# Kernel optimization log

Measured on AMD Instinct MI355X. Metric: run time of the kernel, lower is better.

Reference implementation:

```python
import jax, jax.numpy as jnp
import numpy as np
import math

B, S, D, H = 64, 512, 768, 12
HS = D // H  # head size = 64


def setup_inputs() -> dict:
    key = jax.random.key(0)
    ks = jax.random.split(key, 8)
    scale = 1.0 / math.sqrt(D)
    return {
        "from_tensor": jax.random.normal(ks[0], (B, S, D), jnp.float32),
        "to_tensor": jax.random.normal(ks[1], (B, S, D), jnp.float32),
        "Wq": jax.random.normal(ks[2], (D, D), jnp.float32) * scale,
        "bq": jax.random.normal(ks[3], (D,), jnp.float32) * 0.02,
        "Wk": jax.random.normal(ks[4], (D, D), jnp.float32) * scale,
        "bk": jax.random.normal(ks[5], (D,), jnp.float32) * 0.02,
        "Wv": jax.random.normal(ks[6], (D, D), jnp.float32) * scale,
        "bv": jax.random.normal(ks[7], (D,), jnp.float32) * 0.02,
    }


def _split_heads(x):
    # [B, S, D] -> [B, H, S, HS]
    return x.reshape(B, S, H, HS).transpose(0, 2, 1, 3)


def reference(from_tensor, to_tensor, Wq, bq, Wk, bk, Wv, bv):
    q = _split_heads(from_tensor @ Wq + bq)
    k = _split_heads(to_tensor @ Wk + bk)
    v = _split_heads(to_tensor @ Wv + bv)
    scores = jnp.einsum("bhqd,bhkd->bhqk", q, k) / math.sqrt(HS)
    probs = jax.nn.softmax(scores, axis=-1)
    out = jnp.einsum("bhqk,bhkd->bhqd", probs, v)
    return out.transpose(0, 2, 1, 3).reshape(B, S, D)
```

## Files before the change

### kernel.cpp

```cpp
#include <hip/hip_runtime.h>
#include <hip/hip_bf16.h>

#define GAS __attribute__((address_space(1)))
#define LAS __attribute__((address_space(3)))

typedef __attribute__((ext_vector_type(8))) short   bf16x8;
typedef __attribute__((ext_vector_type(4))) float   f32x4;
typedef __attribute__((ext_vector_type(16))) float  f32x16;
typedef __attribute__((ext_vector_type(4))) float   f4;
typedef __attribute__((ext_vector_type(8))) short   s8v;
typedef __attribute__((ext_vector_type(2))) unsigned int u32x2;
typedef __attribute__((ext_vector_type(4))) unsigned int u32x4;

#define NB  64
#define NS  512
#define ND  768
#define NH  12
#define NHS 64
#define NM  (NB*NS)
#define NBH (NB*NH)

#define QSCALE 0.18033688011112042f

__device__ __forceinline__ unsigned short f2bf(float x){
  unsigned int u = __float_as_uint(x);
  u += 0x7fffu + ((u >> 16) & 1u);
  return (unsigned short)(u >> 16);
}

__device__ __forceinline__ f32x4 mfma16(bf16x8 a, bf16x8 b, f32x4 c){
  return __builtin_amdgcn_mfma_f32_16x16x32_bf16(a, b, c, 0, 0, 0);
}

__device__ __forceinline__ f32x16 mfma32(bf16x8 a, bf16x8 b, f32x16 c){
  return __builtin_amdgcn_mfma_f32_32x32x16_bf16(a, b, c, 0, 0, 0);
}

__device__ __forceinline__ unsigned int cvtpk(float lo, float hi){
  unsigned int r;
  asm("v_cvt_pk_bf16_f32 %0, %1, %2" : "=v"(r) : "v"(lo), "v"(hi));
  return r;
}

__device__ __forceinline__ bf16x8 u2b(u32x4 u){
  union { u32x4 a; bf16x8 b; } c; c.a = u; return c.b;
}

__global__ void cvt_x(const float* __restrict__ from_t, const float* __restrict__ to_t,
                      short* __restrict__ fb, short* __restrict__ tb){
  int v = blockIdx.x * 256 + threadIdx.x;
  const int NG = NM * ND / 8;
  const float* s; short* d;
  if (v < NG){ s = from_t; d = fb; } else { s = to_t; d = tb; v -= NG; }
  f4 a = ((const f4*)s)[(long)v * 2];
  f4 b = ((const f4*)s)[(long)v * 2 + 1];
  s8v o;
  o[0]=(short)f2bf(a[0]); o[1]=(short)f2bf(a[1]); o[2]=(short)f2bf(a[2]); o[3]=(short)f2bf(a[3]);
  o[4]=(short)f2bf(b[0]); o[5]=(short)f2bf(b[1]); o[6]=(short)f2bf(b[2]); o[7]=(short)f2bf(b[3]);
  ((s8v*)d)[v] = o;
}

__global__ void cvt_w(const float* __restrict__ Wq, const float* __restrict__ Wk,
                      const float* __restrict__ Wv, short* __restrict__ Wt){
  int i = blockIdx.x * 256 + threadIdx.x;
  int mat = i / (ND*ND);
  int rem = i - mat * (ND*ND);
  int k = rem / ND;
  int n = rem - k * ND;
  const float* W = (mat == 0) ? Wq : (mat == 1 ? Wk : Wv);
  Wt[(long)mat*ND*ND + (long)n*ND + k] = (short)f2bf(W[rem]);
}

__global__ __launch_bounds__(512, 2)
void qkv_gemm(const short* __restrict__ Xf, const short* __restrict__ Xt,
              const short* __restrict__ Wt,
              const float* __restrict__ bq, const float* __restrict__ bk,
              const float* __restrict__ bv,
              short* __restrict__ Qw, short* __restrict__ Kw, short* __restrict__ Vtw){
  __shared__ short smem[49152];

  int bid = blockIdx.x;
  int wg  = (bid & 7) * 144 + (bid >> 3);
  int mat = wg / 384;
  int r   = wg - mat * 384;
  int mt  = r / 3;
  int nt  = r - mt * 3;

  const short* A  = (mat == 0) ? Xf : Xt;
  const short* Wp = Wt + (long)mat * ND * ND;

  int t_ = threadIdx.x, wv = t_ >> 6, l = t_ & 63, g = l >> 4, c = l & 15;
  int wm = wv >> 2, wn = wv & 3;
  int m0 = mt * 256, n0 = nt * 256;

  short* As[3] = { smem, smem + 8192, smem + 16384 };
  short* Bs[3] = { smem + 24576, smem + 32768, smem + 40960 };

  auto stage = [&](int kt, short* Ab, short* Bb, int ci){
    int chunk = ci * 8 + wv;
    int ch = chunk & 15;
    int idx = ch * 64 + l;
    int row = idx >> 2, slot = idx & 3;
    int kcol = kt * 32 + ((slot ^ ((row >> 1) & 3)) << 3);
    if (chunk < 16){
      const short* gp = A + (long)(m0 + row) * ND + kcol;
      __builtin_amdgcn_global_load_lds((const GAS unsigned int*)gp,
                                       (LAS unsigned int*)(Ab + ch * 512), 16, 0, 0);
    } else {
      const short* gp = Wp + (long)(n0 + row) * ND + kcol;
      __builtin_amdgcn_global_load_lds((const GAS unsigned int*)gp,
                                       (LAS unsigned int*)(Bb + ch * 512), 16, 0, 0);
    }
  };

  f32x4 zero = {0.f, 0.f, 0.f, 0.f};
  f32x4 acc[8][4];
  #pragma unroll
  for (int i = 0; i < 8; ++i)
    #pragma unroll
    for (int j = 0; j < 4; ++j) acc[i][j] = zero;

  #pragma unroll
  for (int ci = 0; ci < 4; ++ci) stage(0, As[0], Bs[0], ci);
  #pragma unroll
  for (int ci = 0; ci < 4; ++ci) stage(1, As[1], Bs[1], ci);

  auto step = [&](const short* Asl, const short* Bsl, short* An, short* Bn, int t){
    if (t == 23) asm volatile("s_waitcnt vmcnt(0)" ::: "memory");
    else         asm volatile("s_waitcnt vmcnt(4)" ::: "memory");
    __builtin_amdgcn_s_barrier();
    bf16x8 af[8], bfr[4];
    #pragma unroll
    for (int ms = 0; ms < 4; ++ms){
      int row = wm * 128 + ms * 16 + c;
      af[ms] = *(const bf16x8*)(Asl + row * 32 + ((g ^ ((row >> 1) & 3)) << 3));
    }
    if (t < 22) stage(t + 2, An, Bn, 0);
    #pragma unroll
    for (int ns = 0; ns < 4; ++ns){
      int row = wn * 64 + ns * 16 + c;
      bfr[ns] = *(const bf16x8*)(Bsl + row * 32 + ((g ^ ((row >> 1) & 3)) << 3));
    }
    if (t < 22) stage(t + 2, An, Bn, 1);
    #pragma unroll
    for (int ms = 4; ms < 8; ++ms){
      int row = wm * 128 + ms * 16 + c;
      af[ms] = *(const bf16x8*)(Asl + row * 32 + ((g ^ ((row >> 1) & 3)) << 3));
    }
    if (t < 22){ stage(t + 2, An, Bn, 2); stage(t + 2, An, Bn, 3); }
    __builtin_amdgcn_s_setprio(1);
    #pragma unroll
    for (int ms = 0; ms < 8; ++ms)
      #pragma unroll
      for (int ns = 0; ns < 4; ++ns)
        acc[ms][ns] = mfma16(af[ms], bfr[ns], acc[ms][ns]);
    __builtin_amdgcn_s_setprio(0);
  };

  for (int it = 0; it < 8; ++it){
    int t = it * 3;
    step(As[0], Bs[0], As[2], Bs[2], t);
    step(As[1], Bs[1], As[0], Bs[0], t + 1);
    step(As[2], Bs[2], As[1], Bs[1], t + 2);
  }

  __builtin_amdgcn_s_barrier();

  int n0g = n0 + wn * 64;
  const float* bias = (mat == 0) ? bq : (mat == 1 ? bk : bv);
  float bb[4];
  #pragma unroll
  for (int ns = 0; ns < 4; ++ns) bb[ns] = bias[n0g + ns * 16 + c];
  short* chunk = smem + wv * 4096;
  int hq = n0g >> 6;

  if (mat < 2){
    short* O = (mat == 0) ? Qw : Kw;
    float scl = (mat == 0) ? QSCALE : 1.0f;
    #pragma unroll
    for (int sp = 0; sp < 2; ++sp){
      #pragma unroll
      for (int msl = 0; msl < 4; ++msl){
        #pragma unroll
        for (int ns = 0; ns < 4; ++ns){
          int col = ns * 16 + c;
          #pragma unroll
          for (int i = 0; i < 4; ++i){
            int row = msl * 16 + g * 4 + i;
            chunk[row * 64 + (((col >> 3) ^ (row & 7)) << 3) + (col & 7)] =
                (short)f2bf((acc[sp * 4 + msl][ns][i] + bb[ns]) * scl);
          }
        }
      }
      asm volatile("s_waitcnt lgkmcnt(0)" ::: "memory");
      __builtin_amdgcn_sched_barrier(0);
      #pragma unroll
      for (int rr = 0; rr < 8; ++rr){
        int row = rr * 8 + (l >> 3);
        int slot = l & 7;
        bf16x8 v = *(const bf16x8*)(chunk + row * 64 + ((slot ^ (row & 7)) << 3));
        int m = m0 + wm * 128 + sp * 64 + row;
        int b = m >> 9, s2 = m & 511;
        *(bf16x8*)(O + (((long)(b * NH + hq) * NS + s2) << 6) + slot * 8) = v;
      }
      if (sp == 0){ asm volatile("s_waitcnt lgkmcnt(0)" ::: "memory"); }
    }
  } else {
    #pragma unroll
    for (int sp = 0; sp < 2; ++sp){
      #pragma unroll
      for (int msl = 0; msl < 4; ++msl){
        #pragma unroll
        for (int ns = 0; ns < 4; ++ns){
          int hs = ns * 16 + c;
          #pragma unroll
          for (int i = 0; i < 4; ++i){
            int col = msl * 16 + g * 4 + i;
            chunk[hs * 64 + (((col >> 3) ^ (hs & 7)) << 3) + (col & 7)] =
                (short)f2bf(acc[sp * 4 + msl][ns][i] + bb[ns]);
          }
        }
      }
      asm volatile("s_waitcnt lgkmcnt(0)" ::: "memory");
      __builtin_amdgcn_sched_barrier(0);
      int mbase = m0 + wm * 128 + sp * 64;
      int b = mbase >> 9, s0 = mbase & 511;
      #pragma unroll
      for (int rr = 0; rr < 8; ++rr){
        int hs = rr * 8 + (l >> 3);
        int slot = l & 7;
        bf16x8 v = *(const bf16x8*)(chunk + hs * 64 + ((slot ^ (hs & 7)) << 3));
        *(bf16x8*)(Vtw + (long)((b * NH + hq) * 64 + hs) * NS + s0 + slot * 8) = v;
      }
      if (sp == 0){ asm volatile("s_waitcnt lgkmcnt(0)" ::: "memory"); }
    }
  }
}

__global__ __launch_bounds__(512, 1)
void attn_kernel(const short* __restrict__ Qw, const short* __restrict__ Kw,
                 const short* __restrict__ Vtw, float* __restrict__ out){
  extern __shared__ char smem[];
  short* Ks = (short*)smem;
  short* Vs = (short*)(smem + 65536);

  int bh = blockIdx.x;
  int t = threadIdx.x, wv = t >> 6, l = t & 63;
  int lam = l & 31, hi = l >> 5;
  int r7 = lam & 7;

  const short* Kb = Kw  + (long)bh * NS * NHS;
  const short* Vb = Vtw + (long)bh * NS * NHS;

  #pragma unroll
  for (int it = 0; it < 8; ++it){
    int chunk = it * 8 + wv;
    {
      int idx = chunk * 64 + l;
      int row = idx >> 3, slot = idx & 7;
      const short* gk = Kb + row * 64 + ((slot ^ (row & 7)) * 8);
      __builtin_amdgcn_global_load_lds((const GAS unsigned int*)gk,
                                       (LAS unsigned int*)(Ks + chunk * 512), 16, 0, 0);
    }
    {
      int row = chunk, slot = l;
      const short* gv = Vb + (long)row * NS + (((slot & 56) | ((slot & 7) ^ (row & 7))) * 8);
      __builtin_amdgcn_global_load_lds((const GAS unsigned int*)gv,
                                       (LAS unsigned int*)(Vs + chunk * 512), 16, 0, 0);
    }
  }
  __syncthreads();

  int b = bh / NH, h = bh - b * NH;
  float* outb = out + (long)b * NS * ND + (long)h * 64;

  for (int qt = 0; qt < 2; ++qt){
    int q0 = wv * 64 + qt * 32;
    const short* Qb = Qw + (((long)bh * NS + q0 + lam) << 6) + hi * 8;
    bf16x8 qf[4];
    #pragma unroll
    for (int dk = 0; dk < 4; ++dk) qf[dk] = *(const bf16x8*)(Qb + dk * 16);

    f32x16 o0, o1;
    #pragma unroll
    for (int j = 0; j < 16; ++j){ o0[j] = 0.f; o1[j] = 0.f; }
    float m_run = -1e30f, lsum = 0.f;

    #pragma unroll
    for (int ch = 0; ch < 16; ++ch){
      f32x16 s;
      #pragma unroll
      for (int j = 0; j < 16; ++j) s[j] = 0.f;
      const char* kbase = (const char*)Ks + (ch * 32 + lam) * 128;
      #pragma unroll
      for (int dk = 0; dk < 4; ++dk){
        bf16x8 kf = *(const bf16x8*)(kbase + (((hi + 2 * dk) ^ r7) << 4));
        s = mfma32(kf, qf[dk], s);
      }

      float t8[8], t4[4];
      #pragma unroll
      for (int j = 0; j < 8; ++j) t8[j] = fmaxf(s[j], s[j + 8]);
      #pragma unroll
      for (int j = 0; j < 4; ++j) t4[j] = fmaxf(t8[j], t8[j + 4]);
      float m1 = fmaxf(fmaxf(t4[0], t4[1]), fmaxf(t4[2], t4[3]));
      float pmax = fmaxf(m1, __shfl_xor(m1, 32));
      if (__any(pmax > m_run + 8.0f)){
        float mnew = fmaxf(m_run, pmax);
        float cf = exp2f(m_run - mnew);
        lsum *= cf;
        #pragma unroll
        for (int j = 0; j < 16; ++j){ o0[j] *= cf; o1[j] *= cf; }
        m_run = mnew;
      }
      float p[16];
      #pragma unroll
      for (int j = 0; j < 16; ++j) p[j] = exp2f(s[j] - m_run);
      float a8[8], a4[4];
      #pragma unroll
      for (int j = 0; j < 8; ++j) a8[j] = p[j] + p[j + 8];
      #pragma unroll
      for (int j = 0; j < 4; ++j) a4[j] = a8[j] + a8[j + 4];
      lsum += (a4[0] + a4[1]) + (a4[2] + a4[3]);

      unsigned int w[8];
      #pragma unroll
      for (int rr = 0; rr < 8; ++rr) w[rr] = cvtpk(p[2 * rr], p[2 * rr + 1]);
      unsigned int y0 = (unsigned int)__shfl_xor((int)(hi ? w[0] : w[2]), 32);
      unsigned int y1 = (unsigned int)__shfl_xor((int)(hi ? w[1] : w[3]), 32);
      unsigned int y2 = (unsigned int)__shfl_xor((int)(hi ? w[4] : w[6]), 32);
      unsigned int y3 = (unsigned int)__shfl_xor((int)(hi ? w[5] : w[7]), 32);
      u32x4 fa, fb;
      if (hi){
        fa[0] = y0;   fa[1] = y1;   fa[2] = w[2]; fa[3] = w[3];
        fb[0] = y2;   fb[1] = y3;   fb[2] = w[6]; fb[3] = w[7];
      } else {
        fa[0] = w[0]; fa[1] = w[1]; fa[2] = y0;   fa[3] = y1;
        fb[0] = w[4]; fb[1] = w[5]; fb[2] = y2;   fb[3] = y3;
      }
      bf16x8 pa = u2b(fa), pb = u2b(fb);

      const char* vb0 = (const char*)Vs + lam * 1024;
      const char* vb1 = (const char*)Vs + (32 + lam) * 1024;
      int sl0 = ch * 4 + hi, sl1 = ch * 4 + 2 + hi;
      int sw0 = ((sl0 & 56) | ((sl0 & 7) ^ r7)) << 4;
      int sw1 = ((sl1 & 56) | ((sl1 & 7) ^ r7)) << 4;
      bf16x8 v00 = *(const bf16x8*)(vb0 + sw0);
      bf16x8 v01 = *(const bf16x8*)(vb0 + sw1);
      bf16x8 v10 = *(const bf16x8*)(vb1 + sw0);
      bf16x8 v11 = *(const bf16x8*)(vb1 + sw1);
      o0 = mfma32(v00, pa, o0);
      o0 = mfma32(v01, pb, o0);
      o1 = mfma32(v10, pa, o1);
      o1 = mfma32(v11, pb, o1);
    }

    float lt = lsum + __shfl_xor(lsum, 32);
    float invl = 1.0f / lt;
    float* orow = outb + (long)(q0 + lam) * ND;
    #pragma unroll
    for (int r = 0; r < 4; ++r){
      f4 u0, u1;
      #pragma unroll
      for (int jj = 0; jj < 4; ++jj){
        u0[jj] = o0[4 * r + jj] * invl;
        u1[jj] = o1[4 * r + jj] * invl;
      }
      *(f4*)(orow + 4 * hi + 8 * r)      = u0;
      *(f4*)(orow + 32 + 4 * hi + 8 * r) = u1;
    }
  }
}

extern "C" void kernel_launch(void* const* d_in, const int* in_sizes, int n_in,
                              void* d_out, int out_size, void* d_ws, size_t ws_size,
                              hipStream_t stream){
  const float* from_t = (const float*)d_in[0];
  const float* to_t   = (const float*)d_in[1];
  const float* Wq = (const float*)d_in[2];
  const float* bq = (const float*)d_in[3];
  const float* Wk = (const float*)d_in[4];
  const float* bk = (const float*)d_in[5];
  const float* Wv = (const float*)d_in[6];
  const float* bv = (const float*)d_in[7];

  short* fb  = (short*)d_ws;
  short* tb  = fb  + 25165824;
  short* Wt  = tb  + 25165824;
  short* Qw  = Wt  + 1769472;
  short* Kw  = Qw  + 25165824;
  short* Vtw = Kw  + 25165824;

  cvt_x<<<24576, 256, 0, stream>>>(from_t, to_t, fb, tb);
  cvt_w<<<6912, 256, 0, stream>>>(Wq, Wk, Wv, Wt);
  qkv_gemm<<<1152, 512, 0, stream>>>(fb, tb, Wt, bq, bk, bv, Qw, Kw, Vtw);
  attn_kernel<<<768, 512, 131072, stream>>>(Qw, Kw, Vtw, (float*)d_out);
}
```

Before: 330.9 us.

## Restructure QKV GEMM mainloop into 4-stage ping-pong pipeline with split MFMA phases

Replaces the 3-buffer LDS pipeline with a 4-slot ring (LDS grows to 128KB), prefetching three k-tiles ahead. Each k-step is split into two halves: loads of half the A fragments, issue of the A or B tile prefetch, then 16 MFMAs, with barriers between phases in a ping-pong style. The aim is to hide global-load latency and overlap LDS reads with MFMA, at the cost of more barriers per step and a larger LDS footprint that may limit blocks per CU.

Result: no change. 330.2 us (-0.2%).

```diff
diff --git a/kernel.cpp b/kernel.cpp
--- a/kernel.cpp
+++ b/kernel.cpp
@@ -77,7 +77,7 @@
               const float* __restrict__ bq, const float* __restrict__ bk,
               const float* __restrict__ bv,
               short* __restrict__ Qw, short* __restrict__ Kw, short* __restrict__ Vtw){
-  __shared__ short smem[49152];
+  __shared__ short smem[65536];
 
   int bid = blockIdx.x;
   int wg  = (bid & 7) * 144 + (bid >> 3);
@@ -93,23 +93,18 @@
   int wm = wv >> 2, wn = wv & 3;
   int m0 = mt * 256, n0 = nt * 256;
 
-  short* As[3] = { smem, smem + 8192, smem + 16384 };
-  short* Bs[3] = { smem + 24576, smem + 32768, smem + 40960 };
-
-  auto stage = [&](int kt, short* Ab, short* Bb, int ci){
-    int chunk = ci * 8 + wv;
-    int ch = chunk & 15;
-    int idx = ch * 64 + l;
-    int row = idx >> 2, slot = idx & 3;
-    int kcol = kt * 32 + ((slot ^ ((row >> 1) & 3)) << 3);
-    if (chunk < 16){
-      const short* gp = A + (long)(m0 + row) * ND + kcol;
+  auto stageH = [&](int kt2, int hf){
+    int sl = kt2 & 3;
+    short* base = smem + (hf ? 32768 : 0) + sl * 8192;
+    const short* src = hf ? Wp : A;
+    int r0 = hf ? n0 : m0;
+    #pragma unroll
+    for (int j = 0; j < 2; ++j){
+      int idx = j * 512 + t_;
+      int row = idx >> 2, slot = idx & 3;
+      const short* gp = src + (long)(r0 + row) * ND + kt2 * 32 + ((slot ^ ((row >> 1) & 3)) << 3);
       __builtin_amdgcn_global_load_lds((const GAS unsigned int*)gp,
-                                       (LAS unsigned int*)(Ab + ch * 512), 16, 0, 0);
-    } else {
-      const short* gp = Wp + (long)(n0 + row) * ND + kcol;
-      __builtin_amdgcn_global_load_lds((const GAS unsigned int*)gp,
-                                       (LAS unsigned int*)(Bb + ch * 512), 16, 0, 0);
+                                       (LAS unsigned int*)(base + idx * 8), 16, 0, 0);
     }
   };
 
@@ -120,51 +115,63 @@
     #pragma unroll
     for (int j = 0; j < 4; ++j) acc[i][j] = zero;
 
-  #pragma unroll
-  for (int ci = 0; ci < 4; ++ci) stage(0, As[0], Bs[0], ci);
-  #pragma unroll
-  for (int ci = 0; ci < 4; ++ci) stage(1, As[1], Bs[1], ci);
-
-  auto step = [&](const short* Asl, const short* Bsl, short* An, short* Bn, int t){
-    if (t == 23) asm volatile("s_waitcnt vmcnt(0)" ::: "memory");
-    else         asm volatile("s_waitcnt vmcnt(4)" ::: "memory");
-    __builtin_amdgcn_s_barrier();
-    bf16x8 af[8], bfr[4];
-    #pragma unroll
-    for (int ms = 0; ms < 4; ++ms){
-      int row = wm * 128 + ms * 16 + c;
-      af[ms] = *(const bf16x8*)(Asl + row * 32 + ((g ^ ((row >> 1) & 3)) << 3));
-    }
-    if (t < 22) stage(t + 2, An, Bn, 0);
+  stageH(0, 0); stageH(0, 1);
+  stageH(1, 0); stageH(1, 1);
+  stageH(2, 0); stageH(2, 1);
+  asm volatile("s_waitcnt vmcnt(8)" ::: "memory");
+  __builtin_amdgcn_s_barrier();
+
+  bf16x8 bfr[4];
+  for (int kt = 0; kt < 24; ++kt){
+    int sl = kt & 3;
+    const short* Asl = smem + sl * 8192;
+    const short* Bsl = smem + 32768 + sl * 8192;
+
+    bf16x8 af[4];
+    #pragma unroll
+    for (int i = 0; i < 4; ++i){
+      int row = wm * 128 + i * 16 + c;
+      af[i] = *(const bf16x8*)(Asl + row * 32 + ((g ^ ((row >> 1) & 3)) << 3));
+    }
     #pragma unroll
     for (int ns = 0; ns < 4; ++ns){
       int row = wn * 64 + ns * 16 + c;
       bfr[ns] = *(const bf16x8*)(Bsl + row * 32 + ((g ^ ((row >> 1) & 3)) << 3));
     }
-    if (t < 22) stage(t + 2, An, Bn, 1);
-    #pragma unroll
-    for (int ms = 4; ms < 8; ++ms){
-      int row = wm * 128 + ms * 16 + c;
-      af[ms] = *(const bf16x8*)(Asl + row * 32 + ((g ^ ((row >> 1) & 3)) << 3));
-    }
-    if (t < 22){ stage(t + 2, An, Bn, 2); stage(t + 2, An, Bn, 3); }
+    if (kt < 21) stageH(kt + 3, 0);
+    __builtin_amdgcn_s_barrier();
+    asm volatile("s_waitcnt lgkmcnt(0)" ::: "memory");
+    __builtin_amdgcn_sched_barrier(0);
     __builtin_amdgcn_s_setprio(1);
     #pragma unroll
-    for (int ms = 0; ms < 8; ++ms)
+    for (int i = 0; i < 4; ++i)
       #pragma unroll
       for (int ns = 0; ns < 4; ++ns)
-        acc[ms][ns] = mfma16(af[ms], bfr[ns], acc[ms][ns]);
+        acc[i][ns] = mfma16(af[i], bfr[ns], acc[i][ns]);
     __builtin_amdgcn_s_setprio(0);
-  };
-
-  for (int it = 0; it < 8; ++it){
-    int t = it * 3;
-    step(As[0], Bs[0], As[2], Bs[2], t);
-    step(As[1], Bs[1], As[0], Bs[0], t + 1);
-    step(As[2], Bs[2], As[1], Bs[1], t + 2);
+    __builtin_amdgcn_s_barrier();
+
+    #pragma unroll
+    for (int i = 0; i < 4; ++i){
+      int row = wm * 128 + (4 + i) * 16 + c;
+      af[i] = *(const bf16x8*)(Asl + row * 32 + ((g ^ ((row >> 1) & 3)) << 3));
+    }
+    if (kt < 21) stageH(kt + 3, 1);
+    __builtin_amdgcn_s_barrier();
+    asm volatile("s_waitcnt lgkmcnt(0)" ::: "memory");
+    __builtin_amdgcn_sched_barrier(0);
+    __builtin_amdgcn_s_setprio(1);
+    #pragma unroll
+    for (int i = 0; i < 4; ++i)
+      #pragma unroll
+      for (int ns = 0; ns < 4; ++ns)
+        acc[4 + i][ns] = mfma16(af[i], bfr[ns], acc[4 + i][ns]);
+    __builtin_amdgcn_s_setprio(0);
+    if (kt <= 20)      asm volatile("s_waitcnt vmcnt(8)" ::: "memory");
+    else if (kt == 21) asm volatile("s_waitcnt vmcnt(4)" ::: "memory");
+    else if (kt == 22) asm volatile("s_waitcnt vmcnt(0)" ::: "memory");
+    __builtin_amdgcn_s_barrier();
   }
-
-  __builtin_amdgcn_s_barrier();
 
   int n0g = n0 + wn * 64;
   const float* bias = (mat == 0) ? bq : (mat == 1 ? bk : bv);
```

## Shrink QKV GEMM tiles to 128x128, single-buffer K=64 steps, merge conversion kernels

Applied to the files above, without the earlier changes.

Merges the activation and weight bf16 conversion kernels into one launch. Rewrites the QKV projection GEMM from 256x256 tiles with 512 threads and a triple-buffered K=32 pipeline into 128x128 tiles with 256 threads. The new GEMM uses a single 32KB LDS buffer with K=64 steps and two syncthreads per step, launching four times as many blocks. This trades data reuse and load/compute overlap for higher occupancy and a simpler schedule, and risks exposing global-load latency because loads are no longer prefetched ahead of compute.

Result: slower. 375.2 us (+13.4%).

```diff
diff --git a/kernel.cpp b/kernel.cpp
--- a/kernel.cpp
+++ b/kernel.cpp
@@ -9,7 +9,6 @@
 typedef __attribute__((ext_vector_type(16))) float  f32x16;
 typedef __attribute__((ext_vector_type(4))) float   f4;
 typedef __attribute__((ext_vector_type(8))) short   s8v;
-typedef __attribute__((ext_vector_type(2))) unsigned int u32x2;
 typedef __attribute__((ext_vector_type(4))) unsigned int u32x4;
 
 #define NB  64
@@ -18,7 +17,6 @@
 #define NH  12
 #define NHS 64
 #define NM  (NB*NS)
-#define NBH (NB*NH)
 
 #define QSCALE 0.18033688011112042f
 
@@ -46,125 +44,106 @@
   union { u32x4 a; bf16x8 b; } c; c.a = u; return c.b;
 }
 
-__global__ void cvt_x(const float* __restrict__ from_t, const float* __restrict__ to_t,
-                      short* __restrict__ fb, short* __restrict__ tb){
-  int v = blockIdx.x * 256 + threadIdx.x;
-  const int NG = NM * ND / 8;
-  const float* s; short* d;
-  if (v < NG){ s = from_t; d = fb; } else { s = to_t; d = tb; v -= NG; }
-  f4 a = ((const f4*)s)[(long)v * 2];
-  f4 b = ((const f4*)s)[(long)v * 2 + 1];
-  s8v o;
-  o[0]=(short)f2bf(a[0]); o[1]=(short)f2bf(a[1]); o[2]=(short)f2bf(a[2]); o[3]=(short)f2bf(a[3]);
-  o[4]=(short)f2bf(b[0]); o[5]=(short)f2bf(b[1]); o[6]=(short)f2bf(b[2]); o[7]=(short)f2bf(b[3]);
-  ((s8v*)d)[v] = o;
-}
-
-__global__ void cvt_w(const float* __restrict__ Wq, const float* __restrict__ Wk,
-                      const float* __restrict__ Wv, short* __restrict__ Wt){
-  int i = blockIdx.x * 256 + threadIdx.x;
-  int mat = i / (ND*ND);
-  int rem = i - mat * (ND*ND);
-  int k = rem / ND;
-  int n = rem - k * ND;
-  const float* W = (mat == 0) ? Wq : (mat == 1 ? Wk : Wv);
-  Wt[(long)mat*ND*ND + (long)n*ND + k] = (short)f2bf(W[rem]);
-}
-
-__global__ __launch_bounds__(512, 2)
+__global__ void cvt_all(const float* __restrict__ from_t, const float* __restrict__ to_t,
+                        const float* __restrict__ Wq, const float* __restrict__ Wk,
+                        const float* __restrict__ Wv,
+                        short* __restrict__ fb, short* __restrict__ tb,
+                        short* __restrict__ Wt){
+  int bid = blockIdx.x;
+  if (bid < 24576){
+    int v = bid * 256 + threadIdx.x;
+    const int NG = NM * ND / 8;
+    const float* s; short* d;
+    if (v < NG){ s = from_t; d = fb; } else { s = to_t; d = tb; v -= NG; }
+    f4 a = ((const f4*)s)[(long)v * 2];
+    f4 b = ((const f4*)s)[(long)v * 2 + 1];
+    s8v o;
+    o[0]=(short)f2bf(a[0]); o[1]=(short)f2bf(a[1]); o[2]=(short)f2bf(a[2]); o[3]=(short)f2bf(a[3]);
+    o[4]=(short)f2bf(b[0]); o[5]=(short)f2bf(b[1]); o[6]=(short)f2bf(b[2]); o[7]=(short)f2bf(b[3]);
+    ((s8v*)d)[v] = o;
+  } else {
+    int i = (bid - 24576) * 256 + threadIdx.x;
+    int mat = i / (ND*ND);
+    int rem = i - mat * (ND*ND);
+    int k = rem / ND;
+    int n = rem - k * ND;
+    const float* W = (mat == 0) ? Wq : (mat == 1 ? Wk : Wv);
+    Wt[(long)mat*ND*ND + (long)n*ND + k] = (short)f2bf(W[rem]);
+  }
+}
+
+__global__ __launch_bounds__(256)
 void qkv_gemm(const short* __restrict__ Xf, const short* __restrict__ Xt,
               const short* __restrict__ Wt,
               const float* __restrict__ bq, const float* __restrict__ bk,
               const float* __restrict__ bv,
               short* __restrict__ Qw, short* __restrict__ Kw, short* __restrict__ Vtw){
-  __shared__ short smem[49152];
+  __shared__ short smem[16384];
 
   int bid = blockIdx.x;
-  int wg  = (bid & 7) * 144 + (bid >> 3);
-  int mat = wg / 384;
-  int r   = wg - mat * 384;
-  int mt  = r / 3;
-  int nt  = r - mt * 3;
+  int wg  = (bid & 7) * 576 + (bid >> 3);
+  int mat = wg / 1536;
+  int r   = wg - mat * 1536;
+  int mt  = r / 6;
+  int nt  = r - mt * 6;
 
   const short* A  = (mat == 0) ? Xf : Xt;
   const short* Wp = Wt + (long)mat * ND * ND;
 
   int t_ = threadIdx.x, wv = t_ >> 6, l = t_ & 63, g = l >> 4, c = l & 15;
-  int wm = wv >> 2, wn = wv & 3;
-  int m0 = mt * 256, n0 = nt * 256;
-
-  short* As[3] = { smem, smem + 8192, smem + 16384 };
-  short* Bs[3] = { smem + 24576, smem + 32768, smem + 40960 };
-
-  auto stage = [&](int kt, short* Ab, short* Bb, int ci){
-    int chunk = ci * 8 + wv;
-    int ch = chunk & 15;
-    int idx = ch * 64 + l;
-    int row = idx >> 2, slot = idx & 3;
-    int kcol = kt * 32 + ((slot ^ ((row >> 1) & 3)) << 3);
-    if (chunk < 16){
-      const short* gp = A + (long)(m0 + row) * ND + kcol;
-      __builtin_amdgcn_global_load_lds((const GAS unsigned int*)gp,
-                                       (LAS unsigned int*)(Ab + ch * 512), 16, 0, 0);
-    } else {
-      const short* gp = Wp + (long)(n0 + row) * ND + kcol;
-      __builtin_amdgcn_global_load_lds((const GAS unsigned int*)gp,
-                                       (LAS unsigned int*)(Bb + ch * 512), 16, 0, 0);
+  int wm = wv >> 1, wn = wv & 1;
+  int m0 = mt * 128, n0 = nt * 128;
+
+  auto stage = [&](int kt){
+    #pragma unroll
+    for (int it = 0; it < 4; ++it){
+      int idx = it * 256 + t_;
+      int row = idx >> 3, slot = idx & 7;
+      int kc = kt * 64 + ((slot ^ (row & 7)) << 3);
+      const short* ga = A + (long)(m0 + row) * ND + kc;
+      __builtin_amdgcn_global_load_lds((const GAS unsigned int*)ga,
+                                       (LAS unsigned int*)(smem + idx * 8), 16, 0, 0);
+      const short* gb = Wp + (long)(n0 + row) * ND + kc;
+      __builtin_amdgcn_global_load_lds((const GAS unsigned int*)gb,
+                                       (LAS unsigned int*)(smem + 8192 + idx * 8), 16, 0, 0);
     }
   };
 
   f32x4 zero = {0.f, 0.f, 0.f, 0.f};
-  f32x4 acc[8][4];
+  f32x4 acc[4][4];
   #pragma unroll
-  for (int i = 0; i < 8; ++i)
+  for (int i = 0; i < 4; ++i)
     #pragma unroll
     for (int j = 0; j < 4; ++j) acc[i][j] = zero;
 
-  #pragma unroll
-  for (int ci = 0; ci < 4; ++ci) stage(0, As[0], Bs[0], ci);
-  #pragma unroll
-  for (int ci = 0; ci < 4; ++ci) stage(1, As[1], Bs[1], ci);
-
-  auto step = [&](const short* Asl, const short* Bsl, short* An, short* Bn, int t){
-    if (t == 23) asm volatile("s_waitcnt vmcnt(0)" ::: "memory");
-    else         asm volatile("s_waitcnt vmcnt(4)" ::: "memory");
-    __builtin_amdgcn_s_barrier();
-    bf16x8 af[8], bfr[4];
+  stage(0);
+  for (int kt = 0; kt < 12; ++kt){
+    __syncthreads();
+    bf16x8 af[4][2], bfr[4][2];
     #pragma unroll
     for (int ms = 0; ms < 4; ++ms){
-      int row = wm * 128 + ms * 16 + c;
-      af[ms] = *(const bf16x8*)(Asl + row * 32 + ((g ^ ((row >> 1) & 3)) << 3));
-    }
-    if (t < 22) stage(t + 2, An, Bn, 0);
+      int row = wm * 64 + ms * 16 + c;
+      #pragma unroll
+      for (int kk = 0; kk < 2; ++kk)
+        af[ms][kk] = *(const bf16x8*)(smem + row * 64 + (((kk * 4 + g) ^ (row & 7)) << 3));
+    }
     #pragma unroll
     for (int ns = 0; ns < 4; ++ns){
       int row = wn * 64 + ns * 16 + c;
-      bfr[ns] = *(const bf16x8*)(Bsl + row * 32 + ((g ^ ((row >> 1) & 3)) << 3));
-    }
-    if (t < 22) stage(t + 2, An, Bn, 1);
-    #pragma unroll
-    for (int ms = 4; ms < 8; ++ms){
-      int row = wm * 128 + ms * 16 + c;
-      af[ms] = *(const bf16x8*)(Asl + row * 32 + ((g ^ ((row >> 1) & 3)) << 3));
-    }
-    if (t < 22){ stage(t + 2, An, Bn, 2); stage(t + 2, An, Bn, 3); }
-    __builtin_amdgcn_s_setprio(1);
-    #pragma unroll
-    for (int ms = 0; ms < 8; ++ms)
-      #pragma unroll
-      for (int ns = 0; ns < 4; ++ns)
-        acc[ms][ns] = mfma16(af[ms], bfr[ns], acc[ms][ns]);
-    __builtin_amdgcn_s_setprio(0);
-  };
-
-  for (int it = 0; it < 8; ++it){
-    int t = it * 3;
-    step(As[0], Bs[0], As[2], Bs[2], t);
-    step(As[1], Bs[1], As[0], Bs[0], t + 1);
-    step(As[2], Bs[2], As[1], Bs[1], t + 2);
-  }
-
-  __builtin_amdgcn_s_barrier();
+      #pragma unroll
+      for (int kk = 0; kk < 2; ++kk)
+        bfr[ns][kk] = *(const bf16x8*)(smem + 8192 + row * 64 + (((kk * 4 + g) ^ (row & 7)) << 3));
+    }
+    #pragma unroll
+    for (int kk = 0; kk < 2; ++kk)
+      #pragma unroll
+      for (int ms = 0; ms < 4; ++ms)
+        #pragma unroll
+        for (int ns = 0; ns < 4; ++ns)
+          acc[ms][ns] = mfma16(af[ms][kk], bfr[ns][kk], acc[ms][ns]);
+    __syncthreads();
+    if (kt < 11) stage(kt + 1);
+  }
 
   int n0g = n0 + wn * 64;
   const float* bias = (mat == 0) ? bq : (mat == 1 ? bk : bv);
@@ -173,66 +152,56 @@
   for (int ns = 0; ns < 4; ++ns) bb[ns] = bias[n0g + ns * 16 + c];
   short* chunk = smem + wv * 4096;
   int hq = n0g >> 6;
+  int mbase = m0 + wm * 64;
+  int b = mbase >> 9, s0 = mbase & 511;
 
   if (mat < 2){
     short* O = (mat == 0) ? Qw : Kw;
     float scl = (mat == 0) ? QSCALE : 1.0f;
     #pragma unroll
-    for (int sp = 0; sp < 2; ++sp){
-      #pragma unroll
-      for (int msl = 0; msl < 4; ++msl){
+    for (int msl = 0; msl < 4; ++msl){
+      #pragma unroll
+      for (int ns = 0; ns < 4; ++ns){
+        int col = ns * 16 + c;
         #pragma unroll
-        for (int ns = 0; ns < 4; ++ns){
-          int col = ns * 16 + c;
-          #pragma unroll
-          for (int i = 0; i < 4; ++i){
-            int row = msl * 16 + g * 4 + i;
-            chunk[row * 64 + (((col >> 3) ^ (row & 7)) << 3) + (col & 7)] =
-                (short)f2bf((acc[sp * 4 + msl][ns][i] + bb[ns]) * scl);
-          }
+        for (int i = 0; i < 4; ++i){
+          int row = msl * 16 + g * 4 + i;
+          chunk[row * 64 + (((col >> 3) ^ (row & 7)) << 3) + (col & 7)] =
+              (short)f2bf((acc[msl][ns][i] + bb[ns]) * scl);
         }
       }
-      asm volatile("s_waitcnt lgkmcnt(0)" ::: "memory");
-      __builtin_amdgcn_sched_barrier(0);
-      #pragma unroll
-      for (int rr = 0; rr < 8; ++rr){
-        int row = rr * 8 + (l >> 3);
-        int slot = l & 7;
-        bf16x8 v = *(const bf16x8*)(chunk + row * 64 + ((slot ^ (row & 7)) << 3));
-        int m = m0 + wm * 128 + sp * 64 + row;
-        int b = m >> 9, s2 = m & 511;
-        *(bf16x8*)(O + (((long)(b * NH + hq) * NS + s2) << 6) + slot * 8) = v;
-      }
-      if (sp == 0){ asm volatile("s_waitcnt lgkmcnt(0)" ::: "memory"); }
+    }
+    asm volatile("s_waitcnt lgkmcnt(0)" ::: "memory");
+    __builtin_amdgcn_sched_barrier(0);
+    #pragma unroll
+    for (int rr = 0; rr < 8; ++rr){
+      int row = rr * 8 + (l >> 3);
+      int slot = l & 7;
+      bf16x8 v = *(const bf16x8*)(chunk + row * 64 + ((slot ^ (row & 7)) << 3));
+      *(bf16x8*)(O + (((long)(b * NH + hq) * NS + s0 + row) << 6) + slot * 8) = v;
     }
   } else {
     #pragma unroll
-    for (int sp = 0; sp < 2; ++sp){
-      #pragma unroll
-      for (int msl = 0; msl < 4; ++msl){
+    for (int msl = 0; msl < 4; ++msl){
+      #pragma unroll
+      for (int ns = 0; ns < 4; ++ns){
+        int hs = ns * 16 + c;
         #pragma unroll
-        for (int ns = 0; ns < 4; ++ns){
-          int hs = ns * 16 + c;
-          #pragma unroll
-          for (int i = 0; i < 4; ++i){
-            int col = msl * 16 + g * 4 + i;
-            chunk[hs * 64 + (((col >> 3) ^ (hs & 7)) << 3) + (col & 7)] =
-                (short)f2bf(acc[sp * 4 + msl][ns][i] + bb[ns]);
-          }
+        for (int i = 0; i < 4; ++i){
+          int col = msl * 16 + g * 4 + i;
+          chunk[hs * 64 + (((col >> 3) ^ (hs & 7)) << 3) + (col & 7)] =
+              (short)f2bf(acc[msl][ns][i] + bb[ns]);
         }
       }
-      asm volatile("s_waitcnt lgkmcnt(0)" ::: "memory");
-      __builtin_amdgcn_sched_barrier(0);
-      int mbase = m0 + wm * 128 + sp * 64;
-      int b = mbase >> 9, s0 = mbase & 511;
-      #pragma unroll
-      for (int rr = 0; rr < 8; ++rr){
-        int hs = rr * 8 + (l >> 3);
-        int slot = l & 7;
-        bf16x8 v = *(const bf16x8*)(chunk + hs * 64 + ((slot ^ (hs & 7)) << 3));
-        *(bf16x8*)(Vtw + (long)((b * NH + hq) * 64 + hs) * NS + s0 + slot * 8) = v;
-      }
-      if (sp == 0){ asm volatile("s_waitcnt lgkmcnt(0)" ::: "memory"); }
+    }
+    asm volatile("s_waitcnt lgkmcnt(0)" ::: "memory");
+    __builtin_amdgcn_sched_barrier(0);
+    #pragma unroll
+    for (int rr = 0; rr < 8; ++rr){
+      int hs = rr * 8 + (l >> 3);
+      int slot = l & 7;
+      bf16x8 v = *(const bf16x8*)(chunk + hs * 64 + ((slot ^ (hs & 7)) << 3));
+      *(bf16x8*)(Vtw + (long)((b * NH + hq) * 64 + hs) * NS + s0 + slot * 8) = v;
     }
   }
 }
@@ -391,8 +360,7 @@
   short* Kw  = Qw  + 25165824;
   short* Vtw = Kw  + 25165824;
 
-  cvt_x<<<24576, 256, 0, stream>>>(from_t, to_t, fb, tb);
-  cvt_w<<<6912, 256, 0, stream>>>(Wq, Wk, Wv, Wt);
-  qkv_gemm<<<1152, 512, 0, stream>>>(fb, tb, Wt, bq, bk, bv, Qw, Kw, Vtw);
+  cvt_all<<<31488, 256, 0, stream>>>(from_t, to_t, Wq, Wk, Wv, fb, tb, Wt);
+  qkv_gemm<<<4608, 256, 0, stream>>>(fb, tb, Wt, bq, bk, bv, Qw, Kw, Vtw);
   attn_kernel<<<768, 512, 131072, stream>>>(Qw, Kw, Vtw, (float*)d_out);
 }
```

## Software-pipeline QK^T across chunks in attention and merge conversion kernels

Applied to the files above, without the earlier changes.

In the attention loop, the QK^T MFMAs for the next 32-key chunk are now issued during the current chunk's softmax, using double-buffered K fragments and score registers. This is meant to hide MFMA latency behind the exp and reduction work. The MFMA groups are also wrapped in s_setprio. Separately, the input-conversion and weight-transpose kernels are merged into one launch to remove a launch boundary. The extra buffers raise register pressure, which could reduce occupancy or cause spills.

Measured after the change: 323.1 us. 2.4% less time.

```diff
diff --git a/kernel.cpp b/kernel.cpp
--- a/kernel.cpp
+++ b/kernel.cpp
@@ -18,7 +18,6 @@
 #define NH  12
 #define NHS 64
 #define NM  (NB*NS)
-#define NBH (NB*NH)
 
 #define QSCALE 0.18033688011112042f
 
@@ -46,29 +45,32 @@
   union { u32x4 a; bf16x8 b; } c; c.a = u; return c.b;
 }
 
-__global__ void cvt_x(const float* __restrict__ from_t, const float* __restrict__ to_t,
-                      short* __restrict__ fb, short* __restrict__ tb){
-  int v = blockIdx.x * 256 + threadIdx.x;
-  const int NG = NM * ND / 8;
-  const float* s; short* d;
-  if (v < NG){ s = from_t; d = fb; } else { s = to_t; d = tb; v -= NG; }
-  f4 a = ((const f4*)s)[(long)v * 2];
-  f4 b = ((const f4*)s)[(long)v * 2 + 1];
-  s8v o;
-  o[0]=(short)f2bf(a[0]); o[1]=(short)f2bf(a[1]); o[2]=(short)f2bf(a[2]); o[3]=(short)f2bf(a[3]);
-  o[4]=(short)f2bf(b[0]); o[5]=(short)f2bf(b[1]); o[6]=(short)f2bf(b[2]); o[7]=(short)f2bf(b[3]);
-  ((s8v*)d)[v] = o;
-}
-
-__global__ void cvt_w(const float* __restrict__ Wq, const float* __restrict__ Wk,
-                      const float* __restrict__ Wv, short* __restrict__ Wt){
-  int i = blockIdx.x * 256 + threadIdx.x;
-  int mat = i / (ND*ND);
-  int rem = i - mat * (ND*ND);
-  int k = rem / ND;
-  int n = rem - k * ND;
-  const float* W = (mat == 0) ? Wq : (mat == 1 ? Wk : Wv);
-  Wt[(long)mat*ND*ND + (long)n*ND + k] = (short)f2bf(W[rem]);
+__global__ void cvt_all(const float* __restrict__ from_t, const float* __restrict__ to_t,
+                        const float* __restrict__ Wq, const float* __restrict__ Wk,
+                        const float* __restrict__ Wv,
+                        short* __restrict__ fb, short* __restrict__ tb,
+                        short* __restrict__ Wt){
+  int bid = blockIdx.x;
+  if (bid < 24576){
+    int v = bid * 256 + threadIdx.x;
+    const int NG = NM * ND / 8;
+    const float* s; short* d;
+    if (v < NG){ s = from_t; d = fb; } else { s = to_t; d = tb; v -= NG; }
+    f4 a = ((const f4*)s)[(long)v * 2];
+    f4 b = ((const f4*)s)[(long)v * 2 + 1];
+    s8v o;
+    o[0]=(short)f2bf(a[0]); o[1]=(short)f2bf(a[1]); o[2]=(short)f2bf(a[2]); o[3]=(short)f2bf(a[3]);
+    o[4]=(short)f2bf(b[0]); o[5]=(short)f2bf(b[1]); o[6]=(short)f2bf(b[2]); o[7]=(short)f2bf(b[3]);
+    ((s8v*)d)[v] = o;
+  } else {
+    int i = (bid - 24576) * 256 + threadIdx.x;
+    int mat = i / (ND*ND);
+    int rem = i - mat * (ND*ND);
+    int k = rem / ND;
+    int n = rem - k * ND;
+    const float* W = (mat == 0) ? Wq : (mat == 1 ? Wk : Wv);
+    Wt[(long)mat*ND*ND + (long)n*ND + k] = (short)f2bf(W[rem]);
+  }
 }
 
 __global__ __launch_bounds__(512, 2)
@@ -129,7 +131,7 @@
     if (t == 23) asm volatile("s_waitcnt vmcnt(0)" ::: "memory");
     else         asm volatile("s_waitcnt vmcnt(4)" ::: "memory");
     __builtin_amdgcn_s_barrier();
-    bf16x8 af[8], bfr[4];
+    bf16x8 af[8], bfv[4];
     #pragma unroll
     for (int ms = 0; ms < 4; ++ms){
       int row = wm * 128 + ms * 16 + c;
@@ -139,7 +141,7 @@
     #pragma unroll
     for (int ns = 0; ns < 4; ++ns){
       int row = wn * 64 + ns * 16 + c;
-      bfr[ns] = *(const bf16x8*)(Bsl + row * 32 + ((g ^ ((row >> 1) & 3)) << 3));
+      bfv[ns] = *(const bf16x8*)(Bsl + row * 32 + ((g ^ ((row >> 1) & 3)) << 3));
     }
     if (t < 22) stage(t + 2, An, Bn, 1);
     #pragma unroll
@@ -153,7 +155,7 @@
     for (int ms = 0; ms < 8; ++ms)
       #pragma unroll
       for (int ns = 0; ns < 4; ++ns)
-        acc[ms][ns] = mfma16(af[ms], bfr[ns], acc[ms][ns]);
+        acc[ms][ns] = mfma16(af[ms], bfv[ns], acc[ms][ns]);
     __builtin_amdgcn_s_setprio(0);
   };
 
@@ -286,21 +288,35 @@
     for (int j = 0; j < 16; ++j){ o0[j] = 0.f; o1[j] = 0.f; }
     float m_run = -1e30f, lsum = 0.f;
 
+    f32x16 s2[2];
+    bf16x8 kfr[2][4];
+    {
+      const char* kb = (const char*)Ks + lam * 128;
+      #pragma unroll
+      for (int dk = 0; dk < 4; ++dk)
+        kfr[0][dk] = *(const bf16x8*)(kb + (((hi + 2 * dk) ^ r7) << 4));
+      #pragma unroll
+      for (int j = 0; j < 16; ++j) s2[0][j] = 0.f;
+      __builtin_amdgcn_s_setprio(1);
+      #pragma unroll
+      for (int dk = 0; dk < 4; ++dk) s2[0] = mfma32(kfr[0][dk], qf[dk], s2[0]);
+      __builtin_amdgcn_s_setprio(0);
+    }
+
     #pragma unroll
     for (int ch = 0; ch < 16; ++ch){
-      f32x16 s;
-      #pragma unroll
-      for (int j = 0; j < 16; ++j) s[j] = 0.f;
-      const char* kbase = (const char*)Ks + (ch * 32 + lam) * 128;
-      #pragma unroll
-      for (int dk = 0; dk < 4; ++dk){
-        bf16x8 kf = *(const bf16x8*)(kbase + (((hi + 2 * dk) ^ r7) << 4));
-        s = mfma32(kf, qf[dk], s);
+      const int cur = ch & 1, nxt = cur ^ 1;
+
+      if (ch < 15){
+        const char* kb = (const char*)Ks + ((ch + 1) * 32 + lam) * 128;
+        #pragma unroll
+        for (int dk = 0; dk < 4; ++dk)
+          kfr[nxt][dk] = *(const bf16x8*)(kb + (((hi + 2 * dk) ^ r7) << 4));
       }
 
       float t8[8], t4[4];
       #pragma unroll
-      for (int j = 0; j < 8; ++j) t8[j] = fmaxf(s[j], s[j + 8]);
+      for (int j = 0; j < 8; ++j) t8[j] = fmaxf(s2[cur][j], s2[cur][j + 8]);
       #pragma unroll
       for (int j = 0; j < 4; ++j) t4[j] = fmaxf(t8[j], t8[j + 4]);
       float m1 = fmaxf(fmaxf(t4[0], t4[1]), fmaxf(t4[2], t4[3]));
@@ -315,13 +331,22 @@
       }
       float p[16];
       #pragma unroll
-      for (int j = 0; j < 16; ++j) p[j] = exp2f(s[j] - m_run);
+      for (int j = 0; j < 16; ++j) p[j] = exp2f(s2[cur][j] - m_run);
       float a8[8], a4[4];
       #pragma unroll
       for (int j = 0; j < 8; ++j) a8[j] = p[j] + p[j + 8];
       #pragma unroll
       for (int j = 0; j < 4; ++j) a4[j] = a8[j] + a8[j + 4];
       lsum += (a4[0] + a4[1]) + (a4[2] + a4[3]);
+
+      if (ch < 15){
+        #pragma unroll
+        for (int j = 0; j < 16; ++j) s2[nxt][j] = 0.f;
+        __builtin_amdgcn_s_setprio(1);
+        #pragma unroll
+        for (int dk = 0; dk < 4; ++dk) s2[nxt] = mfma32(kfr[nxt][dk], qf[dk], s2[nxt]);
+        __builtin_amdgcn_s_setprio(0);
+      }
 
       unsigned int w[8];
       #pragma unroll
@@ -349,10 +374,12 @@
       bf16x8 v01 = *(const bf16x8*)(vb0 + sw1);
       bf16x8 v10 = *(const bf16x8*)(vb1 + sw0);
       bf16x8 v11 = *(const bf16x8*)(vb1 + sw1);
+      __builtin_amdgcn_s_setprio(1);
       o0 = mfma32(v00, pa, o0);
       o0 = mfma32(v01, pb, o0);
       o1 = mfma32(v10, pa, o1);
       o1 = mfma32(v11, pb, o1);
+      __builtin_amdgcn_s_setprio(0);
     }
 
     float lt = lsum + __shfl_xor(lsum, 32);
@@ -391,8 +418,7 @@
   short* Kw  = Qw  + 25165824;
   short* Vtw = Kw  + 25165824;
 
-  cvt_x<<<24576, 256, 0, stream>>>(from_t, to_t, fb, tb);
-  cvt_w<<<6912, 256, 0, stream>>>(Wq, Wk, Wv, Wt);
+  cvt_all<<<31488, 256, 0, stream>>>(from_t, to_t, Wq, Wk, Wv, fb, tb, Wt);
   qkv_gemm<<<1152, 512, 0, stream>>>(fb, tb, Wt, bq, bk, bv, Qw, Kw, Vtw);
   attn_kernel<<<768, 512, 131072, stream>>>(Qw, Kw, Vtw, (float*)d_out);
 }
```
